# Performance work log

Hardware: AMD Instinct MI355X
Metric: run time of the kernel (lower is better)

Reference implementation:

```python
import jax, jax.numpy as jnp
import numpy as np

# ---- constants from train_cfg / hardcoded voxel_resolution dicts ----
PC_MIN_X, PC_MIN_Y, PC_MIN_Z = -51.2, -51.2, -5.0
VX, VY, VZ = 0.1, 0.1, 0.2          # voxel_size
OSF = 8                              # out_size_factor
OVERLAP = 0.1                        # gaussian_overlap
MIN_RADIUS = 2
GX, GY, GZ = 128, 128, 2             # heatmap grid (0.8m xy, 4m z steps)
STEP_XY, STEP_Z = 0.4, 1.0           # inner-loop voxel_resolution steps
FMAP = 128                           # feature_map_size = 1024 // 8
EPS32 = float(np.finfo(np.float32).eps)


def gaussian_radius(h, w, min_overlap=OVERLAP):
    # mmdet3d CornerNet-style radius (note the /2, not /(2a))
    b1 = h + w
    c1 = w * h * (1 - min_overlap) / (1 + min_overlap)
    r1 = (b1 + jnp.sqrt(jnp.maximum(b1 * b1 - 4.0 * c1, 0.0))) / 2.0
    b2 = 2.0 * (h + w)
    c2 = (1 - min_overlap) * w * h
    r2 = (b2 + jnp.sqrt(jnp.maximum(b2 * b2 - 16.0 * c2, 0.0))) / 2.0
    b3 = -2.0 * min_overlap * (h + w)
    c3 = (min_overlap - 1.0) * w * h
    r3 = (b3 + jnp.sqrt(jnp.maximum(b3 * b3 - 16.0 * min_overlap * c3, 0.0))) / 2.0
    return jnp.minimum(jnp.minimum(r1, r2), r3)


def build_heatmap(boxes):
    # boxes: [N,9] = (x, y, z_gravity, w, l, h, yaw, vx, vy); labels only route
    # boxes into tasks (task_num=1 here -> all boxes drawn, cls_id unused).
    # N << max_objs*dense_reg (=500) so the cap never triggers.
    x, y, z = boxes[:, 0], boxes[:, 1], boxes[:, 2]
    wf = boxes[:, 3] / VX / OSF   # width  in feature-map units
    lf = boxes[:, 4] / VY / OSF   # length in feature-map units
    hf = boxes[:, 5] / VZ / OSF   # height in feature-map units

    r_xy = gaussian_radius(lf, wf)
    r_z = jnp.maximum(gaussian_radius(lf, hf), gaussian_radius(wf, hf))
    # int() truncation, then clamp by min_radius
    rx = jnp.maximum(MIN_RADIUS, jnp.trunc(r_xy / STEP_XY).astype(jnp.int32))
    ry = rx
    rz = jnp.maximum(MIN_RADIUS, jnp.trunc(r_z / STEP_Z).astype(jnp.int32))

    cx = (x - (-51.2)) / STEP_XY
    cy = (y - (-51.2)) / STEP_XY
    cz = (z - (-5.0)) / STEP_Z
    cxi = cx.astype(jnp.int32)  # trunc-toward-zero, as torch .to(int32)
    cyi = cy.astype(jnp.int32)
    czi = cz.astype(jnp.int32)

    valid = (wf > 0) & (lf > 0) \
        & (cxi >= 0) & (cxi < FMAP) & (cyi >= 0) & (cyi < FMAP) \
        & (czi >= 0) & (czi <= GZ - 1)

    # gaussian sigmas per axis: diameter/6
    sx = (2.0 * rx.astype(jnp.float32) + 1.0) / 6.0
    sy = (2.0 * ry.astype(jnp.float32) + 1.0) / 6.0
    sz = (2.0 * rz.astype(jnp.float32) + 1.0) / 6.0

    dx = jnp.arange(GX, dtype=jnp.int32)[None, :] - cxi[:, None]   # [N,GX]
    dy = jnp.arange(GY, dtype=jnp.int32)[None, :] - cyi[:, None]   # [N,GY]
    dz = jnp.arange(GZ, dtype=jnp.int32)[None, :] - czi[:, None]   # [N,GZ]

    ex = dx.astype(jnp.float32) ** 2 / (2.0 * sx[:, None] ** 2)
    ey = dy.astype(jnp.float32) ** 2 / (2.0 * sy[:, None] ** 2)
    ez = dz.astype(jnp.float32) ** 2 / (2.0 * sz[:, None] ** 2)
    g = jnp.exp(-(ex[:, :, None, None] + ey[:, None, :, None] + ez[:, None, None, :]))
    g = jnp.where(g < EPS32, 0.0, g)  # eps zeroing as in mmdet gaussianND

    win = (jnp.abs(dx) <= rx[:, None])[:, :, None, None] \
        & (jnp.abs(dy) <= ry[:, None])[:, None, :, None] \
        & (jnp.abs(dz) <= rz[:, None])[:, None, None, :]
    g = g * win * valid[:, None, None, None]
    return jnp.max(g, axis=0)  # [GX,GY,GZ]; scatter-max over objects


def lin_resize(x, axis, out_size):
    # 1D linear resize, pytorch trilinear align_corners=False semantics
    in_size = x.shape[axis]
    scale = in_size / out_size
    coords = (jnp.arange(out_size, dtype=jnp.float32) + 0.5) * scale - 0.5
    coords = jnp.clip(coords, 0.0, in_size - 1)
    lo = jnp.floor(coords).astype(jnp.int32)
    hi = jnp.minimum(lo + 1, in_size - 1)
    w = coords - lo.astype(jnp.float32)
    shape = [1] * x.ndim
    shape[axis] = out_size
    w = w.reshape(shape)
    return jnp.take(x, lo, axis=axis) * (1.0 - w) + jnp.take(x, hi, axis=axis) * w


def align(voxels, conv_w, conv_b, out_shape):
    # 1x1x1 Conv3d 64->128 (student has 64 ch), then trilinear interp
    v = jnp.einsum('bcdhw,oc->bodhw', voxels, conv_w) + conv_b[None, :, None, None, None]
    v = lin_resize(v, 2, out_shape[0])
    v = lin_resize(v, 3, out_shape[1])
    v = lin_resize(v, 4, out_shape[2])
    return v


def setup_inputs() -> dict:
    key = jax.random.key(0)
    k1, k2, k3, k4, k5, k6, k7, k8, k9 = jax.random.split(key, 9)
    N = 100
    xy = jax.random.uniform(k1, (N, 2), minval=-50.0, maxval=-1.0)
    z = jax.random.uniform(k2, (N, 1), minval=-5.0, maxval=-3.2)
    dims = jax.random.uniform(k3, (N, 3), minval=1.5, maxval=8.0)
    rest = jax.random.normal(k4, (N, 3)) * 0.1
    gt_bboxes_3d = jnp.concatenate([xy, z, dims, rest], axis=1)  # [N,9]
    gt_labels_3d = jax.random.randint(k5, (N,), 0, 3)
    teacher = jax.random.normal(k6, (1, 128, 2, 128, 128), dtype=jnp.float32)
    student = jax.random.normal(k7, (1, 64, 8, 256, 256), dtype=jnp.float32)
    conv_w = jax.random.normal(k8, (128, 64), dtype=jnp.float32) * 0.125
    conv_b = jax.random.normal(k9, (128,), dtype=jnp.float32) * 0.01
    return {"gt_bboxes_3d": gt_bboxes_3d, "gt_labels_3d": gt_labels_3d,
            "teacher_voxel_feats": teacher, "student_voxel_feats": student,
            "conv_w": conv_w, "conv_b": conv_b}


def reference(gt_bboxes_3d, gt_labels_3d, teacher_voxel_feats, student_voxel_feats, conv_w, conv_b):
    hm = build_heatmap(gt_bboxes_3d)                 # [128,128,2]
    # stack per sample -> [1,B,128,128,2] -> permute(0,1,4,2,3) -> [1,1,2,128,128]
    hm3d = jnp.transpose(hm, (2, 0, 1))[None, None]
    s = align(student_voxel_feats, conv_w, conv_b, teacher_voxel_feats.shape[2:])
    loss = jnp.abs(s - teacher_voxel_feats) * hm3d   # L1, reduction='none'
    loss = loss / (hm3d.sum() + 1e-4)
    return loss * 10.0
```

## Files before the change

kernel.cpp:

```cpp
#include <hip/hip_runtime.h>
#include <math.h>

#define EPS32 1.1920928955078125e-07f
#define NSP 32768
#define HB 128
#define PB 4096


__device__ __forceinline__ float gauss_radius(float h, float w) {
#pragma clang fp contract(off)
    const float mo = 0.1f;
    float b1 = h + w;
    float c1 = w * h * (1.0f - mo) / (1.0f + mo);
    float r1 = (b1 + sqrtf(fmaxf(b1 * b1 - 4.0f * c1, 0.0f))) / 2.0f;
    float b2 = 2.0f * (h + w);
    float c2 = (1.0f - mo) * w * h;
    float r2 = (b2 + sqrtf(fmaxf(b2 * b2 - 16.0f * c2, 0.0f))) / 2.0f;
    float b3 = -2.0f * mo * (h + w);
    float c3 = (mo - 1.0f) * w * h;
    float r3 = (b3 + sqrtf(fmaxf(b3 * b3 - 16.0f * mo * c3, 0.0f))) / 2.0f;
    return fminf(fminf(r1, r2), r3);
}

__global__ void k_stage1(const float* __restrict__ boxes, int N,
                         const float* __restrict__ S,
                         float* __restrict__ P,
                         float* __restrict__ hmv,
                         float* __restrict__ partial) {
    int bx = blockIdx.x;
    int tid = threadIdx.x;

    if (bx < HB) {
        __shared__ int   s_cxi[128], s_cyi[128], s_czi[128], s_rx[128], s_rz[128];
        __shared__ float s_ix[128], s_iz[128];
        if (tid < N) {
#pragma clang fp contract(off)
            int b = tid;
            float x = boxes[b * 9 + 0];
            float y = boxes[b * 9 + 1];
            float z = boxes[b * 9 + 2];
            float wf = boxes[b * 9 + 3] / 0.1f / 8.0f;
            float lf = boxes[b * 9 + 4] / 0.1f / 8.0f;
            float hf = boxes[b * 9 + 5] / 0.2f / 8.0f;
            float r_xy = gauss_radius(lf, wf);
            float r_z  = fmaxf(gauss_radius(lf, hf), gauss_radius(wf, hf));
            int rx = max(2, (int)truncf(r_xy / 0.4f));
            int rz = max(2, (int)truncf(r_z / 1.0f));
            float cx = (x + 51.2f) / 0.4f;
            float cy = (y + 51.2f) / 0.4f;
            float cz = (z + 5.0f) / 1.0f;
            int cxi = (int)cx, cyi = (int)cy, czi = (int)cz;
            int valid = (wf > 0.0f) && (lf > 0.0f) &&
                        cxi >= 0 && cxi < 128 && cyi >= 0 && cyi < 128 &&
                        czi >= 0 && czi <= 1;
            float sx = (2.0f * (float)rx + 1.0f) / 6.0f;
            float sz = (2.0f * (float)rz + 1.0f) / 6.0f;
            s_cxi[b] = cxi;
            s_cyi[b] = cyi;
            s_czi[b] = czi;
            s_rx[b]  = valid ? rx : -1;
            s_rz[b]  = rz;
            s_ix[b]  = 1.0f / (2.0f * sx * sx);
            s_iz[b]  = 1.0f / (2.0f * sz * sz);
        }
        __syncthreads();

        int i = bx * 256 + tid;
        int y = i & 127, x = (i >> 7) & 127, zc = i >> 14;
        float m = 0.0f;
        for (int b = 0; b < N; ++b) {
            int rx = s_rx[b];
            int dx = x - s_cxi[b];
            if (dx > rx || dx < -rx) continue;
            int dy = y - s_cyi[b];
            if (dy > rx || dy < -rx) continue;
            int rz = s_rz[b];
            int dz = zc - s_czi[b];
            if (dz > rz || dz < -rz) continue;
            float e = (float)(dx * dx + dy * dy) * s_ix[b]
                    + (float)(dz * dz) * s_iz[b];
            float g = expf(-e);
            if (g >= EPS32) m = fmaxf(m, g);
        }
        hmv[i] = m;
        __shared__ float sm[256];
        sm[tid] = m;
        __syncthreads();
        for (int s = 128; s > 0; s >>= 1) {
            if (tid < s) sm[tid] += sm[tid + s];
            __syncthreads();
        }
        if (tid == 0) partial[bx] = sm[0];
    } else {
        int j = (bx - HB) * 256 + tid;
        int wp = j & 63;
        int h  = (j >> 6) & 127;
        int d  = (j >> 13) & 1;
        int c  = j >> 14;
        int zl = d ? 5 : 1;
        const float4* S4 = (const float4*)S;
        long base = ((long)(c * 8 + zl) * 256 + 2 * h) * 64 + wp;
        float4 a = S4[base];
        float4 b = S4[base + 64];
        float4 e = S4[base + 16384];
        float4 f = S4[base + 16384 + 64];
        float2 r;
        r.x = (((a.x + a.y) + (b.x + b.y)) + ((e.x + e.y) + (f.x + f.y))) * 0.125f;
        r.y = (((a.z + a.w) + (b.z + b.w)) + ((e.z + e.w) + (f.z + f.w))) * 0.125f;
        ((float2*)P)[j] = r;
    }
}

__global__ __launch_bounds__(256, 2)
void k_final(const float* __restrict__ P, const float* __restrict__ T,
             const float* __restrict__ W, const float* __restrict__ Bb,
             const float* __restrict__ hmv, const float* __restrict__ partial,
             float* __restrict__ out) {
    __shared__ float s_scale;
    int tid = threadIdx.x;
    if (tid < 64) {
        float v = partial[tid] + partial[tid + 64];
        for (int off = 32; off > 0; off >>= 1) v += __shfl_down(v, off, 64);
        if (tid == 0) s_scale = 10.0f / (v + 1e-4f);
    }
    __syncthreads();

    int s = blockIdx.x * 256 + tid;
    int o0 = blockIdx.y * 32;

    const float* Pv = P + s;
    float p[64];
#pragma unroll
    for (int c = 0; c < 64; ++c) p[c] = Pv[c * NSP];

    float hmw = hmv[s] * s_scale;

#pragma unroll 4
    for (int oo = 0; oo < 32; ++oo) {
        int o = o0 + oo;
        const float* w = W + o * 64;
        float acc = Bb[o];
#pragma unroll
        for (int c = 0; c < 64; ++c) acc = fmaf(w[c], p[c], acc);
        out[o * NSP + s] = fabsf(acc - T[o * NSP + s]) * hmw;
    }
}

__global__ __launch_bounds__(256, 2)
void k_final_fused(const float* __restrict__ S, const float* __restrict__ T,
                   const float* __restrict__ W, const float* __restrict__ Bb,
                   const float* __restrict__ hmv, const float* __restrict__ partial,
                   float* __restrict__ out) {
    __shared__ float s_scale;
    int tid = threadIdx.x;
    if (tid < 64) {
        float v = partial[tid] + partial[tid + 64];
        for (int off = 32; off > 0; off >>= 1) v += __shfl_down(v, off, 64);
        if (tid == 0) s_scale = 10.0f / (v + 1e-4f);
    }
    __syncthreads();
    int s = blockIdx.x * 256 + tid;
    int w = s & 127, h = (s >> 7) & 127, d = s >> 14;
    int zl = d ? 5 : 1;
    const float2* S2 = (const float2*)S;
    float p[64];
#pragma unroll
    for (int c = 0; c < 64; ++c) {
        long base = ((long)(c * 8 + zl) * 256 + 2 * h) * 128 + w;
        float2 a = S2[base];
        float2 b = S2[base + 128];
        float2 e = S2[base + 32768];
        float2 f = S2[base + 32768 + 128];
        p[c] = (((a.x + a.y) + (b.x + b.y)) + ((e.x + e.y) + (f.x + f.y))) * 0.125f;
    }
    float hmw = hmv[s] * s_scale;
    int o0 = blockIdx.y * 64;
#pragma unroll 4
    for (int oo = 0; oo < 64; ++oo) {
        int o = o0 + oo;
        const float* wr = W + o * 64;
        float acc = Bb[o];
#pragma unroll
        for (int c = 0; c < 64; ++c) acc = fmaf(wr[c], p[c], acc);
        out[o * NSP + s] = fabsf(acc - T[o * NSP + s]) * hmw;
    }
}

extern "C" void kernel_launch(void* const* d_in, const int* in_sizes, int n_in,
                              void* d_out, int out_size, void* d_ws, size_t ws_size,
                              hipStream_t stream) {
    const float* boxes   = (const float*)d_in[0];
    const float* teacher = (const float*)d_in[2];
    const float* student = (const float*)d_in[3];
    const float* conv_w  = (const float*)d_in[4];
    const float* conv_b  = (const float*)d_in[5];
    float* out = (float*)d_out;

    int N = in_sizes[0] / 9;
    if (N > 128) N = 128;

    float* wsF     = (float*)d_ws;
    float* partial = wsF;
    float* hmv     = wsF + 1024;
    float* pooled  = wsF + 65536;

    const size_t need = (size_t)(65536 + 64 * NSP) * sizeof(float);
    if (ws_size >= need) {
        k_stage1<<<HB + PB, 256, 0, stream>>>(boxes, N, student, pooled, hmv, partial);
        k_final<<<dim3(NSP / 256, 4), 256, 0, stream>>>(pooled, teacher, conv_w, conv_b,
                                                        hmv, partial, out);
    } else {
        k_stage1<<<HB, 256, 0, stream>>>(boxes, N, student,  hmv, hmv, partial);
        k_final_fused<<<dim3(NSP / 256, 2), 256, 0, stream>>>(student, teacher, conv_w, conv_b,
                                                              hmv, partial, out);
    }
}
```

Baseline: 239.0 us.

## Restructure 1x1 conv to accumulate 16 outputs per thread and raise occupancy

The conv loop is inverted. Each thread now streams the 64 pooled input channels once and keeps 16 output accumulators in registers, instead of holding all 64 inputs and looping over 32 or 64 outputs. Launch bounds go to 4 blocks per SM and the grid grows to 8 output-channel groups, so register pressure is lower and there are more waves to hide memory latency. The cost is that pooled (or, in the fused path, student) data is re-read by more blocks along y, which adds memory traffic, mostly absorbed by cache.

```diff
diff --git a/kernel.cpp b/kernel.cpp
--- a/kernel.cpp
+++ b/kernel.cpp
@@ -111,7 +111,7 @@
     }
 }
 
-__global__ __launch_bounds__(256, 2)
+__global__ __launch_bounds__(256, 4)
 void k_final(const float* __restrict__ P, const float* __restrict__ T,
              const float* __restrict__ W, const float* __restrict__ Bb,
              const float* __restrict__ hmv, const float* __restrict__ partial,
@@ -126,23 +126,27 @@
     __syncthreads();
 
     int s = blockIdx.x * 256 + tid;
-    int o0 = blockIdx.y * 32;
+    int o0 = blockIdx.y * 16;
+
+    float acc[16];
+#pragma unroll
+    for (int oo = 0; oo < 16; ++oo) acc[oo] = Bb[o0 + oo];
 
     const float* Pv = P + s;
-    float p[64];
-#pragma unroll
-    for (int c = 0; c < 64; ++c) p[c] = Pv[c * NSP];
+    const float* Wv = W + o0 * 64;
+#pragma unroll 8
+    for (int c = 0; c < 64; ++c) {
+        float pc = Pv[(long)c * NSP];
+#pragma unroll
+        for (int oo = 0; oo < 16; ++oo)
+            acc[oo] = fmaf(Wv[oo * 64 + c], pc, acc[oo]);
+    }
 
     float hmw = hmv[s] * s_scale;
-
-#pragma unroll 4
-    for (int oo = 0; oo < 32; ++oo) {
+#pragma unroll
+    for (int oo = 0; oo < 16; ++oo) {
         int o = o0 + oo;
-        const float* w = W + o * 64;
-        float acc = Bb[o];
-#pragma unroll
-        for (int c = 0; c < 64; ++c) acc = fmaf(w[c], p[c], acc);
-        out[o * NSP + s] = fabsf(acc - T[o * NSP + s]) * hmw;
+        out[(long)o * NSP + s] = fabsf(acc[oo] - T[(long)o * NSP + s]) * hmw;
     }
 }
 
@@ -163,26 +167,28 @@
     int w = s & 127, h = (s >> 7) & 127, d = s >> 14;
     int zl = d ? 5 : 1;
     const float2* S2 = (const float2*)S;
-    float p[64];
-#pragma unroll
+    int o0 = blockIdx.y * 16;
+    float acc[16];
+#pragma unroll
+    for (int oo = 0; oo < 16; ++oo) acc[oo] = Bb[o0 + oo];
+    const float* Wv = W + o0 * 64;
+#pragma unroll 4
     for (int c = 0; c < 64; ++c) {
         long base = ((long)(c * 8 + zl) * 256 + 2 * h) * 128 + w;
         float2 a = S2[base];
         float2 b = S2[base + 128];
         float2 e = S2[base + 32768];
         float2 f = S2[base + 32768 + 128];
-        p[c] = (((a.x + a.y) + (b.x + b.y)) + ((e.x + e.y) + (f.x + f.y))) * 0.125f;
+        float pc = (((a.x + a.y) + (b.x + b.y)) + ((e.x + e.y) + (f.x + f.y))) * 0.125f;
+#pragma unroll
+        for (int oo = 0; oo < 16; ++oo)
+            acc[oo] = fmaf(Wv[oo * 64 + c], pc, acc[oo]);
     }
     float hmw = hmv[s] * s_scale;
-    int o0 = blockIdx.y * 64;
-#pragma unroll 4
-    for (int oo = 0; oo < 64; ++oo) {
+#pragma unroll
+    for (int oo = 0; oo < 16; ++oo) {
         int o = o0 + oo;
-        const float* wr = W + o * 64;
-        float acc = Bb[o];
-#pragma unroll
-        for (int c = 0; c < 64; ++c) acc = fmaf(wr[c], p[c], acc);
-        out[o * NSP + s] = fabsf(acc - T[o * NSP + s]) * hmw;
+        out[(long)o * NSP + s] = fabsf(acc[oo] - T[(long)o * NSP + s]) * hmw;
     }
 }
 
@@ -207,11 +213,11 @@
     const size_t need = (size_t)(65536 + 64 * NSP) * sizeof(float);
     if (ws_size >= need) {
         k_stage1<<<HB + PB, 256, 0, stream>>>(boxes, N, student, pooled, hmv, partial);
-        k_final<<<dim3(NSP / 256, 4), 256, 0, stream>>>(pooled, teacher, conv_w, conv_b,
+        k_final<<<dim3(NSP / 256, 8), 256, 0, stream>>>(pooled, teacher, conv_w, conv_b,
                                                         hmv, partial, out);
     } else {
         k_stage1<<<HB, 256, 0, stream>>>(boxes, N, student,  hmv, hmv, partial);
-        k_final_fused<<<dim3(NSP / 256, 2), 256, 0, stream>>>(student, teacher, conv_w, conv_b,
+        k_final_fused<<<dim3(NSP / 256, 8), 256, 0, stream>>>(student, teacher, conv_w, conv_b,
                                                               hmv, partial, out);
     }
 }
```

Measured after the change: 212.0 us. 1.13x faster.
